# Performance work log

Measured on AMD Instinct MI355X. Metric: run time of the kernel, lower is better.

## Reference

```python
import jax, jax.numpy as jnp
import numpy as np

K = 16          # neighbors (init kwarg k)
LEAK = 0.2      # LeakyReLU slope
EPS = 1e-5      # GroupNorm eps
GROUPS = 4


def knn_idx(coor_k, coor_q, k):
    # coor_* : (B, 3, N); returns (B, Nq, k) indices of k nearest keys per query
    qk = jnp.einsum('bdq,bdk->bqk', coor_q, coor_k)
    q2 = jnp.sum(coor_q * coor_q, axis=1)[:, :, None]
    k2 = jnp.sum(coor_k * coor_k, axis=1)[:, None, :]
    d2 = q2 + k2 - 2.0 * qk                     # (B, Nq, Nk) squared distances
    _, idx = jax.lax.top_k(-d2, k)
    return idx


def gather_feats(x_k, idx):
    # x_k (B, D, Nk), idx (B, Nq, k) -> (B, D, Nq, k)
    feat = jax.vmap(lambda fk, i: fk[i])(jnp.transpose(x_k, (0, 2, 1)), idx)  # (B,Nq,k,D)
    return jnp.transpose(feat, (0, 3, 1, 2))


def graph_feature(coor_q, x_q, coor_k, x_k, k):
    idx = knn_idx(coor_k, coor_q, k)
    feat = gather_feats(x_k, idx)                # (B, D, Nq, k)
    xq = x_q[:, :, :, None]
    return jnp.concatenate([feat - xq, jnp.broadcast_to(xq, feat.shape)], axis=1)


def group_norm(x, gamma, beta):
    B, C, N, Kk = x.shape
    xg = x.reshape(B, GROUPS, C // GROUPS, N, Kk)
    mu = xg.mean(axis=(2, 3, 4), keepdims=True)
    var = xg.var(axis=(2, 3, 4), keepdims=True)
    xn = ((xg - mu) * jax.lax.rsqrt(var + EPS)).reshape(B, C, N, Kk)
    return xn * gamma[None, :, None, None] + beta[None, :, None, None]


def conv_gn_lrelu(x, w, gamma, beta):
    y = jnp.einsum('oc,bcnk->bonk', w, x)        # 1x1 conv, no bias
    y = group_norm(y, gamma, beta)
    return jnp.where(y > 0, y, LEAK * y)


def fps(xyz, npoint):
    # xyz (B, N, 3) -> (B, npoint) farthest-point-sampling indices, start at 0
    B, N, _ = xyz.shape
    d0 = jnp.full((B, N), 1e10, dtype=xyz.dtype)

    def step(carry, _):
        dist, far = carry
        centroid = jnp.take_along_axis(xyz, far[:, None, None], axis=1)  # (B,1,3)
        d = jnp.sum((xyz - centroid) ** 2, axis=-1)
        dist = jnp.minimum(dist, d)
        nxt = jnp.argmax(dist, axis=-1).astype(jnp.int32)
        return (dist, nxt), far

    far0 = jnp.zeros((B,), dtype=jnp.int32)
    _, idxs = jax.lax.scan(step, (d0, far0), None, length=npoint)
    return jnp.transpose(idxs)                   # (B, npoint)


def fps_downsample(coor, x, num_group):
    # coor (B,3,N), x (B,D,N)
    fidx = fps(jnp.transpose(coor, (0, 2, 1)), num_group)   # (B, num_group)
    comb = jnp.concatenate([coor, x], axis=1)                # (B, 3+D, N)
    new = jax.vmap(lambda c, i: c[:, i])(comb, fidx)         # (B, 3+D, num_group)
    return new[:, :3], new[:, 3:]


def setup_inputs() -> dict:
    key = jax.random.key(0)
    ks = jax.random.split(key, 8)
    B, N = 16, 2048
    return {
        'x': jax.random.normal(ks[0], (B, N, 3), jnp.float32),
        'num0': 512,
        'num1': 128,
        'w_in': jax.random.normal(ks[1], (8, 3), jnp.float32) * 0.3,
        'b_in': jax.random.normal(ks[2], (8,), jnp.float32) * 0.1,
        'w1': jax.random.normal(ks[3], (32, 16), jnp.float32) * 0.2,
        'g1': jnp.ones((32,), jnp.float32), 'be1': jnp.zeros((32,), jnp.float32),
        'w2': jax.random.normal(ks[4], (64, 64), jnp.float32) * 0.12,
        'g2': jnp.ones((64,), jnp.float32), 'be2': jnp.zeros((64,), jnp.float32),
        'w3': jax.random.normal(ks[5], (64, 128), jnp.float32) * 0.09,
        'g3': jnp.ones((64,), jnp.float32), 'be3': jnp.zeros((64,), jnp.float32),
        'w4': jax.random.normal(ks[6], (128, 128), jnp.float32) * 0.09,
        'g4': jnp.ones((128,), jnp.float32), 'be4': jnp.zeros((128,), jnp.float32),
    }


def reference(x, num0, num1, w_in, b_in, w1, g1, be1, w2, g2, be2,
              w3, g3, be3, w4, g4, be4):
    coor = jnp.transpose(x, (0, 2, 1))                       # (B,3,N)
    f = jnp.einsum('oc,bcn->bon', w_in, coor) + b_in[None, :, None]  # (B,8,N)

    f = graph_feature(coor, f, coor, f, K)                   # (B,16,N,K)
    f = conv_gn_lrelu(f, w1, g1, be1).max(axis=-1)           # (B,32,N)

    coor_q, f_q = fps_downsample(coor, f, num0)
    f = graph_feature(coor_q, f_q, coor, f, K)               # (B,64,num0,K)
    f = conv_gn_lrelu(f, w2, g2, be2).max(axis=-1)           # (B,64,num0)
    coor = coor_q

    f = graph_feature(coor, f, coor, f, K)                   # (B,128,num0,K)
    f = conv_gn_lrelu(f, w3, g3, be3).max(axis=-1)           # (B,64,num0)

    coor_q, f_q = fps_downsample(coor, f, num1)
    f = graph_feature(coor_q, f_q, coor, f, K)               # (B,128,num1,K)
    f = conv_gn_lrelu(f, w4, g4, be4).max(axis=-1)           # (B,128,num1)

    return jnp.transpose(coor_q, (0, 2, 1)), jnp.transpose(f, (0, 2, 1))
```

## Files before the change

kernel.cpp:

```cpp
#include <hip/hip_runtime.h>

#define KNN 16
static constexpr int BB = 16;
static constexpr float LEAK = 0.2f;
static constexpr float EPSV = 1e-5f;
typedef unsigned long long u64;

__device__ __forceinline__ void ce_asc(u64 &a, u64 &b) {
  u64 x = a, y = b; bool sw = y < x; a = sw ? y : x; b = sw ? x : y;
}
__device__ __forceinline__ void ce_desc(u64 &a, u64 &b) {
  u64 x = a, y = b; bool sw = x < y; a = sw ? y : x; b = sw ? x : y;
}
__device__ __forceinline__ void bitonic_sort16(u64 *T) {
#pragma unroll
  for (int k = 2; k <= 16; k <<= 1) {
#pragma unroll
    for (int j = k >> 1; j > 0; j >>= 1) {
#pragma unroll
      for (int i = 0; i < 16; ++i) {
        int l = i ^ j;
        if (l > i) {
          if ((i & k) == 0) ce_asc(T[i], T[l]); else ce_desc(T[i], T[l]);
        }
      }
    }
  }
}
__device__ __forceinline__ void merge_sorted16(u64 *R, const u64 *T) {
#pragma unroll
  for (int i = 0; i < 16; ++i) {
    u64 t = T[15 - i];
    R[i] = t < R[i] ? t : R[i];
  }
#pragma unroll
  for (int j = 8; j > 0; j >>= 1) {
#pragma unroll
    for (int i = 0; i < 16; ++i) {
      int l = i ^ j;
      if (l > i) ce_asc(R[i], R[l]);
    }
  }
}
template<int KC>
__device__ __forceinline__ void merge_row(const u64* __restrict__ p, u64* R) {
#pragma unroll
  for (int s = 0; s < 16; ++s) R[s] = p[s];
#pragma unroll
  for (int c = 1; c < KC; ++c) {
    u64 T[16];
#pragma unroll
    for (int s = 0; s < 16; ++s) T[s] = p[(size_t)c*KNN + s];
    merge_sorted16(R, T);
  }
}

__device__ __forceinline__ void f0_dev(const float* __restrict__ x,
    const float* __restrict__ w_in, const float* __restrict__ b_in,
    float* __restrict__ f0, int bid) {
  int i = bid * 256 + threadIdx.x;
  float px = x[i*3+0], py = x[i*3+1], pz = x[i*3+2];
#pragma unroll
  for (int o = 0; o < 8; ++o) {
    f0[i*8+o] = w_in[o*3+0]*px + w_in[o*3+1]*py + w_in[o*3+2]*pz + b_in[o];
  }
}

__device__ void knn_part_dev(const float* __restrict__ qxyz, int Nq,
    const float* __restrict__ kxyz, int Nk, int KC, u64* __restrict__ part,
    char* sm, int bid) {
  float4* keys = (float4*)sm;
  int nqb = (Nq + 255) >> 8;
  int c  = bid % KC;
  int qb = (bid / KC) % nqb;
  int b  = bid / (KC * nqb);
  int nkc = Nk / KC;
  int kbase = c * nkc;
  for (int j = threadIdx.x; j < nkc; j += 256) {
    const float* kp = kxyz + (size_t)(b*Nk + kbase + j)*3;
    float kx = kp[0], ky = kp[1], kz = kp[2];
    keys[j] = make_float4(kx, ky, kz, kx*kx + ky*ky + kz*kz);
  }
  __syncthreads();
  int q = (qb << 8) + threadIdx.x;
  if (q >= Nq) return;
  const float* qp = qxyz + (size_t)(b*Nq + q)*3;
  float qx = qp[0], qy = qp[1], qz = qp[2];
  float q2 = qx*qx + qy*qy + qz*qz;
  u64 R[16];
#pragma unroll
  for (int s = 0; s < 16; ++s) R[s] = 0xFFFFFFFFFFFFFFFFull;
  for (int j0 = 0; j0 < nkc; j0 += 16) {
    u64 T[16];
#pragma unroll
    for (int u = 0; u < 16; ++u) {
      float4 kk = keys[j0 + u];
      float qk = qx*kk.x + qy*kk.y + qz*kk.z;
      float d2 = q2 + kk.w - 2.0f*qk;
      int bb = __float_as_int(d2);
      unsigned k32 = (unsigned)bb ^ (unsigned)((bb >> 31) | 0x80000000);
      T[u] = ((u64)k32 << 32) | (unsigned)(kbase + j0 + u);
    }
    bitonic_sort16(T);
    merge_sorted16(R, T);
  }
  u64* op = part + ((size_t)(b*Nq + q)*KC + c)*KNN;
#pragma unroll
  for (int s = 0; s < KNN; ++s) op[s] = R[s];
}

__device__ __forceinline__ u64 fps_max64(u64 a, u64 b) { return a > b ? a : b; }
template<int CTRL>
__device__ __forceinline__ float fps_dpp_fmax(float v) {
  int nb = __builtin_amdgcn_update_dpp(0, __float_as_int(v), CTRL, 0xF, 0xF, false);
  return fmaxf(v, __int_as_float(nb));
}
template<int P, bool SAVE>
__device__ void fps_seg_dev(const float* __restrict__ xyz, int np,
    int t0, int t1, int* __restrict__ fidx,
    float* __restrict__ g_dl, int* __restrict__ g_far,
    int* __restrict__ inv, float* __restrict__ cq, char* sm, int b) {
  constexpr int NN = P * 256;
  float4* sc  = (float4*)sm;
  int* s_fid  = (int*)(sm + NN*16);
  u64* s_key  = (u64*)(sm + NN*16 + 2048);
  __builtin_amdgcn_s_setprio(1);
  int tid = threadIdx.x;
  int w = tid >> 6, lw = tid & 63;
  float px[P], py[P], pz[P], dl[P];
#pragma unroll
  for (int i = 0; i < P; ++i) {
    int p = tid * P + i;
    const float* pp = xyz + (size_t)(b*NN + p)*3;
    px[i] = pp[0]; py[i] = pp[1]; pz[i] = pp[2];
    sc[p] = make_float4(px[i], py[i], pz[i], 0.f);
  }
  int far;
  if (t0 == 0) {
#pragma unroll
    for (int i = 0; i < P; ++i) dl[i] = 1e10f;
    far = 0;
  } else {
#pragma unroll
    for (int i = 0; i < P; ++i) dl[i] = g_dl[b*NN + tid*P + i];
    far = g_far[b];
  }
  __syncthreads();
  for (int t = t0; t < t1; ++t) {
    if (tid == 0) { fidx[b*np + t] = far; s_fid[t] = far; }
    float4 cc = sc[far];
#pragma unroll
    for (int i = 0; i < P; ++i) {
      float dx = __fsub_rn(px[i], cc.x);
      float dy = __fsub_rn(py[i], cc.y);
      float dz = __fsub_rn(pz[i], cc.z);
      float d = __fadd_rn(__fadd_rn(__fmul_rn(dx,dx), __fmul_rn(dy,dy)), __fmul_rn(dz,dz));
      dl[i] = fminf(dl[i], d);
    }
    float m[P];
#pragma unroll
    for (int i = 0; i < P; ++i) m[i] = dl[i];
#pragma unroll
    for (int st = P/2; st > 0; st >>= 1) {
#pragma unroll
      for (int i = 0; i < P; ++i) if (i < st) m[i] = fmaxf(m[i], m[i + st]);
    }
    float lmax = m[0];
    unsigned msk = 0u;
#pragma unroll
    for (int i = 0; i < P; ++i) msk |= (dl[i] == lmax) ? (1u << i) : 0u;
    int lidx = tid * P + __builtin_ctz(msk);
    float v = lmax;
    v = fps_dpp_fmax<0x111>(v);
    v = fps_dpp_fmax<0x112>(v);
    v = fps_dpp_fmax<0x114>(v);
    v = fps_dpp_fmax<0x118>(v);
    v = fps_dpp_fmax<0x142>(v);
    v = fps_dpp_fmax<0x143>(v);
    float wmax = __int_as_float(__builtin_amdgcn_readlane(__float_as_int(v), 63));
    u64 bal = __ballot(lmax == wmax);
    int l0 = __ffsll((unsigned long long)bal) - 1;
    int wp = __builtin_amdgcn_readlane(lidx, l0);
    int buf = t & 1;
    if (lw == 0)
      s_key[buf*4 + w] = ((u64)__float_as_uint(wmax) << 32) | (unsigned)(~wp);
    __syncthreads();
    u64 best = s_key[buf*4 + 0];
    best = fps_max64(best, s_key[buf*4 + 1]);
    best = fps_max64(best, s_key[buf*4 + 2]);
    best = fps_max64(best, s_key[buf*4 + 3]);
    far = (int)(~(unsigned)(best & 0xFFFFFFFFull));
  }
  if constexpr (SAVE) {
#pragma unroll
    for (int i = 0; i < P; ++i) g_dl[b*NN + tid*P + i] = dl[i];
    if (tid == 0) g_far[b] = far;
  } else {
    __syncthreads();
    for (int j = tid; j < np; j += 256) {
      int p = (j >= t0) ? s_fid[j] : fidx[b*np + j];
      if (inv) inv[b*NN + p] = j;
      float4 c = sc[p];
      float* cp = cq + (size_t)(b*np + j)*3;
      cp[0] = c.x; cp[1] = c.y; cp[2] = c.z;
    }
  }
  __builtin_amdgcn_s_setprio(0);
}

__device__ __forceinline__ void fq1gather_dev(const float* __restrict__ f1,
    const int* __restrict__ fidx1, float* __restrict__ fq1, int bid) {
  int i = bid * 256 + threadIdx.x;
  int b = i >> 9;
  int src = fidx1[i];
  const float4* s = (const float4*)(f1 + (size_t)(b*2048 + src)*32);
  float4* d = (float4*)(fq1 + (size_t)i*32);
#pragma unroll
  for (int c = 0; c < 8; ++c) d[c] = s[c];
}

template<int C, int O, int QB, int KC, int NB>
__device__ void conv_dev(const float* __restrict__ fsrc, int Nsrc,
    const float* __restrict__ fq, int Nq, const u64* __restrict__ part,
    const float* __restrict__ w, float* __restrict__ ym, float* __restrict__ yn,
    double2* __restrict__ pp1, char* sm, int bid) {
  constexpr int Og = O / 4;
  constexpr int C4 = C / 4;
  double* rs  = (double*)sm;
  double* rs2 = rs + 256;
  float* ft   = (float*)(sm + 4096);
  float* fqs  = ft + QB*KNN*C;
  int* s_idx  = (int*)(fqs + QB*C);
  int tid = threadIdx.x;
  int chunk = bid % NB;
  int b = bid / NB;
  int q0 = chunk * QB;
  if (tid < QB) {
    const u64* p = part + (size_t)(b*Nq + q0 + tid)*KC*KNN;
    u64 R[16];
    merge_row<KC>(p, R);
#pragma unroll
    for (int s = 0; s < 16; ++s) s_idx[tid*KNN + s] = (int)(unsigned)(R[s] & 0xFFFFFFFFu);
  } else if (tid >= 64 && tid < 64 + QB*C4) {
    int t = tid - 64;
    int ql = t / C4, c4 = t % C4;
    ((float4*)&fqs[ql*C])[c4] = ((const float4*)(fq + (size_t)(b*Nq + q0 + ql)*C))[c4];
  }
  __syncthreads();
  for (int v = tid; v < QB*KNN*C4; v += 256) {
    int row = v / C4, c4 = v % C4;
    int ql = row / KNN, k = row % KNN;
    int src = s_idx[ql*KNN + k];
    ((float4*)&ft[(ql*KNN + k)*C])[c4] = ((const float4*)(fsrc + (size_t)(b*Nsrc + src)*C))[c4];
  }
  __syncthreads();
  int ql = tid / O, o = tid % O;
  float4 wr4[C4];
  float bs = 0.f;
  const float4* wp4 = (const float4*)(w + (size_t)o*2*C);
#pragma unroll
  for (int c4 = 0; c4 < C4; ++c4) {
    float4 lo = wp4[c4], hi = wp4[C4 + c4];
    float4 fv = ((const float4*)&fqs[ql*C])[c4];
    bs += (hi.x - lo.x) * fv.x;
    bs += (hi.y - lo.y) * fv.y;
    bs += (hi.z - lo.z) * fv.z;
    bs += (hi.w - lo.w) * fv.w;
    wr4[c4] = lo;
  }
  float mx = -3.4e38f, mn = 3.4e38f;
  double s = 0.0, s2 = 0.0;
  for (int k = 0; k < KNN; ++k) {
    float acc = bs;
    const float4* fv = (const float4*)&ft[(ql*KNN + k)*C];
#pragma unroll
    for (int c4 = 0; c4 < C4; ++c4) {
      float4 v = fv[c4];
      acc += wr4[c4].x*v.x; acc += wr4[c4].y*v.y;
      acc += wr4[c4].z*v.z; acc += wr4[c4].w*v.w;
    }
    mx = fmaxf(mx, acc);
    mn = fminf(mn, acc);
    s += acc;
    s2 += (double)acc * (double)acc;
  }
  size_t oidx = (size_t)(b*Nq + q0 + ql)*O + o;
  ym[oidx] = mx;
  yn[oidx] = mn;
  rs[tid] = s; rs2[tid] = s2;
  __syncthreads();
#pragma unroll
  for (int st = QB/2; st > 0; st >>= 1) {
    if (ql < st) { rs[tid] += rs[tid + st*O]; rs2[tid] += rs2[tid + st*O]; }
    __syncthreads();
  }
#pragma unroll
  for (int st = Og/2; st > 0; st >>= 1) {
    if (tid < O && (o % Og) < st) { rs[tid] += rs[tid + st]; rs2[tid] += rs2[tid + st]; }
    __syncthreads();
  }
  if (tid < O && (o % Og) == 0) {
    int g = o / Og;
    pp1[((size_t)b*NB + chunk)*4 + g] = make_double2(rs[tid], rs2[tid]);
  }
}

template<int O, int NB, int FCH, int NQ, int NSEL>
__device__ void fin_dev(const float* __restrict__ ym, const float* __restrict__ yn,
    const double2* __restrict__ pp1, const float* __restrict__ gamma,
    const float* __restrict__ beta, float* __restrict__ fout,
    const int* __restrict__ inv, float* __restrict__ fqout, char* sm, int bid) {
  constexpr int Og = O / 4;
  double* red  = (double*)sm;
  double* red2 = red + 64;
  float* s_mu  = (float*)(red2 + 64);
  float* s_rsv = s_mu + 4;
  int tid = threadIdx.x;
  int b = bid / FCH;
  int f = bid % FCH;
  if (tid < 64) {
    int g = tid >> 4, j = tid & 15;
    double s = 0.0, s2 = 0.0;
    for (int c = j; c < NB; c += 16) {
      double2 v = pp1[((size_t)b*NB + c)*4 + g];
      s += v.x; s2 += v.y;
    }
    red[tid] = s; red2[tid] = s2;
  }
  __syncthreads();
#pragma unroll
  for (int st = 8; st > 0; st >>= 1) {
    if (tid < 64 && (tid & 15) < st) { red[tid] += red[tid+st]; red2[tid] += red2[tid+st]; }
    __syncthreads();
  }
  if (tid < 4) {
    double cnt = (double)Og * (double)NQ * (double)KNN;
    double mu = red[tid*16] / cnt;
    double var = red2[tid*16] / cnt - mu*mu;
    s_mu[tid] = (float)mu;
    s_rsv[tid] = 1.0f / sqrtf((float)var + EPSV);
  }
  __syncthreads();
  constexpr int PER = NQ * O / FCH;
  int e0 = f * PER;
  for (int e = e0 + tid; e < e0 + PER; e += 256) {
    int q = e / O, o = e % O;
    int g = o / Og;
    size_t idx = (size_t)(b*NQ + q)*O + o;
    float ga = gamma[o], be = beta[o];
    float ysel = (ga >= 0.f) ? ym[idx] : yn[idx];
    float xn = (ysel - s_mu[g]) * s_rsv[g];
    float yv = xn*ga + be;
    yv = yv > 0.f ? yv : LEAK*yv;
    fout[idx] = yv;
    if constexpr (NSEL > 0) {
      int j = inv[b*NQ + q];
      if (j >= 0) fqout[(size_t)(b*NSEL + j)*O + o] = yv;
    }
  }
}

__global__ __launch_bounds__(256) void fusedA_kernel(const float* __restrict__ x,
    const float* __restrict__ w_in, const float* __restrict__ b_in,
    float* __restrict__ f0, u64* __restrict__ part, int* __restrict__ fidx1,
    float* __restrict__ g_dl, int* __restrict__ g_far) {
  extern __shared__ char sm[];
  int bid = blockIdx.x;
  if (bid < 16)        fps_seg_dev<8,true>(x, 512, 0, 280, fidx1, g_dl, g_far, nullptr, nullptr, sm, bid);
  else if (bid < 1040) knn_part_dev(x, 2048, x, 2048, 8, part, sm, bid - 16);
  else                 f0_dev(x, w_in, b_in, f0, bid - 1040);
}

__global__ __launch_bounds__(256) void conv1_kernel(const float* __restrict__ x,
    int* __restrict__ fidx1, float* __restrict__ g_dl, int* __restrict__ g_far,
    const float* __restrict__ f0, const u64* __restrict__ part,
    const float* __restrict__ w1, float* __restrict__ ym, float* __restrict__ yn,
    double2* __restrict__ pp1) {
  extern __shared__ char sm[];
  int bid = blockIdx.x;
  if (bid < 16) fps_seg_dev<8,true>(x, 512, 280, 460, fidx1, g_dl, g_far, nullptr, nullptr, sm, bid);
  else          conv_dev<8,32,8,8,256>(f0, 2048, f0, 2048, part, w1, ym, yn, pp1, sm, bid - 16);
}

__global__ __launch_bounds__(256) void fin1_kernel(const float* __restrict__ x,
    int* __restrict__ fidx1, float* __restrict__ g_dl, int* __restrict__ g_far,
    float* __restrict__ cq1,
    const float* __restrict__ ym, const float* __restrict__ yn,
    const double2* __restrict__ pp1, const float* __restrict__ g1,
    const float* __restrict__ be1, float* __restrict__ f1) {
  extern __shared__ char sm[];
  int bid = blockIdx.x;
  if (bid < 16) fps_seg_dev<8,false>(x, 512, 460, 512, fidx1, g_dl, g_far, nullptr, cq1, sm, bid);
  else          fin_dev<32,256,32,2048,0>(ym, yn, pp1, g1, be1, f1, nullptr, nullptr, sm, bid - 16);
}

__global__ __launch_bounds__(256) void fusedB_kernel(const float* __restrict__ cq1,
    const float* __restrict__ x, u64* __restrict__ part2, u64* __restrict__ part3,
    int* __restrict__ fidx2, float* __restrict__ g_dl, int* __restrict__ g_far,
    int* __restrict__ inv2, const float* __restrict__ f1, const int* __restrict__ fidx1,
    float* __restrict__ fq1) {
  extern __shared__ char sm[];
  int bid = blockIdx.x;
  if (bid < 16) {
    fps_seg_dev<2,true>(cq1, 128, 0, 100, fidx2, g_dl, g_far, nullptr, nullptr, sm, bid);
  } else if (bid < 272) {
    if (bid < 48) inv2[(bid - 16)*256 + threadIdx.x] = -1;
    knn_part_dev(cq1, 512, x, 2048, 8, part2, sm, bid - 16);
  } else if (bid < 528) {
    knn_part_dev(cq1, 512, cq1, 512, 8, part3, sm, bid - 272);
  } else {
    fq1gather_dev(f1, fidx1, fq1, bid - 528);
  }
}

__global__ __launch_bounds__(256) void conv2_kernel(const float* __restrict__ cq1,
    int* __restrict__ fidx2, float* __restrict__ g_dl, int* __restrict__ g_far,
    int* __restrict__ inv2, float* __restrict__ cq2,
    const float* __restrict__ f1, const float* __restrict__ fq1,
    const u64* __restrict__ part2, const float* __restrict__ w2,
    float* __restrict__ ym, float* __restrict__ yn, double2* __restrict__ pp1) {
  extern __shared__ char sm[];
  int bid = blockIdx.x;
  if (bid < 16) fps_seg_dev<2,false>(cq1, 128, 100, 128, fidx2, g_dl, g_far, inv2, cq2, sm, bid);
  else          conv_dev<32,64,4,8,128>(f1, 2048, fq1, 512, part2, w2, ym, yn, pp1, sm, bid - 16);
}

__global__ __launch_bounds__(256) void fin2_kernel(const float* __restrict__ ym,
    const float* __restrict__ yn, const double2* __restrict__ pp1,
    const float* __restrict__ g2, const float* __restrict__ be2,
    float* __restrict__ f2) {
  extern __shared__ char sm[];
  fin_dev<64,128,16,512,0>(ym, yn, pp1, g2, be2, f2, nullptr, nullptr, sm, blockIdx.x);
}

__global__ __launch_bounds__(256) void conv3k4_kernel(const float* __restrict__ cq2,
    const float* __restrict__ cq1, u64* __restrict__ part4,
    const float* __restrict__ f2, const u64* __restrict__ part3,
    const float* __restrict__ w3, float* __restrict__ ym, float* __restrict__ yn,
    double2* __restrict__ pp1) {
  extern __shared__ char sm[];
  int bid = blockIdx.x;
  if (bid < 128) knn_part_dev(cq2, 128, cq1, 512, 8, part4, sm, bid);
  else           conv_dev<64,64,4,8,128>(f2, 512, f2, 512, part3, w3, ym, yn, pp1, sm, bid - 128);
}

__global__ __launch_bounds__(256) void fin3_kernel(const float* __restrict__ ym,
    const float* __restrict__ yn, const double2* __restrict__ pp1,
    const float* __restrict__ g3, const float* __restrict__ be3,
    float* __restrict__ f3, const int* __restrict__ inv2, float* __restrict__ fq2) {
  extern __shared__ char sm[];
  fin_dev<64,128,16,512,128>(ym, yn, pp1, g3, be3, f3, inv2, fq2, sm, blockIdx.x);
}

__global__ __launch_bounds__(256) void conv4_kernel(const float* __restrict__ f3,
    const float* __restrict__ fq2, const u64* __restrict__ part4,
    const float* __restrict__ w4, float* __restrict__ ym, float* __restrict__ yn,
    double2* __restrict__ pp1) {
  extern __shared__ char sm[];
  conv_dev<64,128,2,8,64>(f3, 512, fq2, 128, part4, w4, ym, yn, pp1, sm, blockIdx.x);
}

__global__ __launch_bounds__(256) void fin4_kernel(const float* __restrict__ ym,
    const float* __restrict__ yn, const double2* __restrict__ pp1,
    const float* __restrict__ g4, const float* __restrict__ be4,
    float* __restrict__ f4) {
  extern __shared__ char sm[];
  fin_dev<128,64,8,128,0>(ym, yn, pp1, g4, be4, f4, nullptr, nullptr, sm, blockIdx.x);
}

extern "C" void kernel_launch(void* const* d_in, const int* in_sizes, int n_in,
                              void* d_out, int out_size, void* d_ws, size_t ws_size,
                              hipStream_t stream) {
  const float* x    = (const float*)d_in[0];
  const float* w_in = (const float*)d_in[3];
  const float* b_in = (const float*)d_in[4];
  const float* w1 = (const float*)d_in[5];
  const float* g1 = (const float*)d_in[6];
  const float* be1= (const float*)d_in[7];
  const float* w2 = (const float*)d_in[8];
  const float* g2 = (const float*)d_in[9];
  const float* be2= (const float*)d_in[10];
  const float* w3 = (const float*)d_in[11];
  const float* g3 = (const float*)d_in[12];
  const float* be3= (const float*)d_in[13];
  const float* w4 = (const float*)d_in[14];
  const float* g4 = (const float*)d_in[15];
  const float* be4= (const float*)d_in[16];
  float* out = (float*)d_out;
  (void)in_sizes; (void)n_in; (void)out_size; (void)ws_size;

  char* ws = (char*)d_ws;
  size_t off = 0;
  auto alloc = [&](size_t count) {
    void* p = ws + off;
    off += (count * 4 + 255) & ~(size_t)255;
    return p;
  };
  float* f0    = (float*)alloc(16*2048*8);
  float* f1    = (float*)alloc(16*2048*32);
  float* f2    = (float*)alloc(16*512*64);
  float* f3    = (float*)alloc(16*512*64);
  float* fq1   = (float*)alloc(16*512*32);
  float* fq2   = (float*)alloc(16*128*64);
  float* cq1   = (float*)alloc(16*512*3);
  float* ym    = (float*)alloc(16*2048*32);
  float* yn    = (float*)alloc(16*2048*32);
  double2* pp1 = (double2*)alloc(16*256*4*4);
  int* fidx1   = (int*)alloc(16*512);
  int* fidx2   = (int*)alloc(16*128);
  int* inv2    = (int*)alloc(16*512);
  float* g_dl1 = (float*)alloc(16*2048);
  int* g_far1  = (int*)alloc(16);
  float* g_dl2 = (float*)alloc(16*512);
  int* g_far2  = (int*)alloc(16);
  u64* part1 = (u64*)alloc((size_t)2 * 16*2048*8*16);
  u64* part2 = part1;
  u64* part3 = part1 + (size_t)16*512*8*16;
  u64* part4 = part1 + (size_t)2*16*512*8*16;

  float* cq2 = out;
  float* f4  = out + 16*128*3;

  constexpr size_t SM_F1  = 2048*16 + 2048 + 64;
  constexpr size_t SM_F2  = 512*16 + 2048 + 64;
  constexpr size_t SM_KNN = 4096;
  constexpr size_t SM_C1  = 4096 + 8*KNN*8*4 + 8*8*4 + 8*KNN*4;
  constexpr size_t SM_C2  = 4096 + 4*KNN*32*4 + 4*32*4 + 4*KNN*4;
  constexpr size_t SM_C3  = 4096 + 4*KNN*64*4 + 4*64*4 + 4*KNN*4;
  constexpr size_t SM_C4  = 4096 + 2*KNN*64*4 + 2*64*4 + 2*KNN*4;
  constexpr size_t SM_FIN = 1056;
  auto mx2 = [](size_t a, size_t b) { return a > b ? a : b; };

  fusedA_kernel<<<1168, 256, mx2(SM_F1, SM_KNN), stream>>>(x, w_in, b_in, f0, part1, fidx1, g_dl1, g_far1);
  conv1_kernel<<<4112, 256, mx2(SM_F1, SM_C1), stream>>>(x, fidx1, g_dl1, g_far1, f0, part1, w1, ym, yn, pp1);
  fin1_kernel<<<528, 256, mx2(SM_F1, SM_FIN), stream>>>(x, fidx1, g_dl1, g_far1, cq1, ym, yn, pp1, g1, be1, f1);

  fusedB_kernel<<<560, 256, mx2(SM_F2, SM_KNN), stream>>>(cq1, x, part2, part3, fidx2, g_dl2, g_far2, inv2, f1, fidx1, fq1);
  conv2_kernel<<<2064, 256, mx2(SM_F2, SM_C2), stream>>>(cq1, fidx2, g_dl2, g_far2, inv2, cq2, f1, fq1, part2, w2, ym, yn, pp1);
  fin2_kernel<<<256, 256, SM_FIN, stream>>>(ym, yn, pp1, g2, be2, f2);

  conv3k4_kernel<<<2176, 256, mx2(SM_KNN, SM_C3), stream>>>(cq2, cq1, part4, f2, part3, w3, ym, yn, pp1);
  fin3_kernel<<<256, 256, SM_FIN, stream>>>(ym, yn, pp1, g3, be3, f3, inv2, fq2);

  conv4_kernel<<<1024, 256, SM_C4, stream>>>(f3, fq2, part4, w4, ym, yn, pp1);
  fin4_kernel<<<128, 256, SM_FIN, stream>>>(ym, yn, pp1, g4, be4, f4);
}
```

Before: 470.5 us.

## Run second FPS stage in a single wavefront without block barriers

```diff
diff --git a/kernel.cpp b/kernel.cpp
--- a/kernel.cpp
+++ b/kernel.cpp
@@ -115,11 +115,14 @@
   int nb = __builtin_amdgcn_update_dpp(0, __float_as_int(v), CTRL, 0xF, 0xF, false);
   return fmaxf(v, __int_as_float(nb));
 }
+__device__ __forceinline__ float rl_f(float v, int l) {
+  return __int_as_float(__builtin_amdgcn_readlane(__float_as_int(v), l));
+}
 template<int P, bool SAVE>
 __device__ void fps_seg_dev(const float* __restrict__ xyz, int np,
     int t0, int t1, int* __restrict__ fidx,
     float* __restrict__ g_dl, int* __restrict__ g_far,
-    int* __restrict__ inv, float* __restrict__ cq, char* sm, int b) {
+    float* __restrict__ cq, char* sm, int b) {
   constexpr int NN = P * 256;
   float4* sc  = (float4*)sm;
   int* s_fid  = (int*)(sm + NN*16);
@@ -147,7 +150,7 @@
   }
   __syncthreads();
   for (int t = t0; t < t1; ++t) {
-    if (tid == 0) { fidx[b*np + t] = far; s_fid[t] = far; }
+    if (tid == 0) s_fid[t] = far;
     float4 cc = sc[far];
 #pragma unroll
     for (int i = 0; i < P; ++i) {
@@ -177,7 +180,7 @@
     v = fps_dpp_fmax<0x118>(v);
     v = fps_dpp_fmax<0x142>(v);
     v = fps_dpp_fmax<0x143>(v);
-    float wmax = __int_as_float(__builtin_amdgcn_readlane(__float_as_int(v), 63));
+    float wmax = rl_f(v, 63);
     u64 bal = __ballot(lmax == wmax);
     int l0 = __ffsll((unsigned long long)bal) - 1;
     int wp = __builtin_amdgcn_readlane(lidx, l0);
@@ -191,18 +194,107 @@
     best = fps_max64(best, s_key[buf*4 + 3]);
     far = (int)(~(unsigned)(best & 0xFFFFFFFFull));
   }
+  for (int t = t0 + tid; t < t1; t += 256) fidx[b*np + t] = s_fid[t];
   if constexpr (SAVE) {
 #pragma unroll
     for (int i = 0; i < P; ++i) g_dl[b*NN + tid*P + i] = dl[i];
     if (tid == 0) g_far[b] = far;
   } else {
-    __syncthreads();
     for (int j = tid; j < np; j += 256) {
       int p = (j >= t0) ? s_fid[j] : fidx[b*np + j];
-      if (inv) inv[b*NN + p] = j;
       float4 c = sc[p];
       float* cp = cq + (size_t)(b*np + j)*3;
       cp[0] = c.x; cp[1] = c.y; cp[2] = c.z;
+    }
+  }
+  __builtin_amdgcn_s_setprio(0);
+}
+
+template<int P, bool SAVE>
+__device__ void fps2_wave_dev(const float* __restrict__ xyz, int np,
+    int t0, int t1, int* __restrict__ fidx,
+    float* __restrict__ g_dl, int* __restrict__ g_far,
+    int* __restrict__ inv, float* __restrict__ cq, char* sm, int b) {
+  constexpr int NN = P * 64;
+  int* s_fid = (int*)sm;
+  __builtin_amdgcn_s_setprio(1);
+  int l = threadIdx.x;
+  float px[P], py[P], pz[P], dl[P];
+#pragma unroll
+  for (int i = 0; i < P; ++i) {
+    int p = l * P + i;
+    const float* pp = xyz + (size_t)(b*NN + p)*3;
+    px[i] = pp[0]; py[i] = pp[1]; pz[i] = pp[2];
+  }
+  int far;
+  if (t0 == 0) {
+#pragma unroll
+    for (int i = 0; i < P; ++i) dl[i] = 1e10f;
+    far = 0;
+  } else {
+#pragma unroll
+    for (int i = 0; i < P; ++i) dl[i] = g_dl[b*NN + l*P + i];
+    far = g_far[b];
+  }
+  const float* fp = xyz + (size_t)(b*NN + far)*3;
+  float ccx = fp[0], ccy = fp[1], ccz = fp[2];
+  for (int t = t0; t < t1; ++t) {
+    if (l == 0) s_fid[t] = far;
+#pragma unroll
+    for (int i = 0; i < P; ++i) {
+      float dx = __fsub_rn(px[i], ccx);
+      float dy = __fsub_rn(py[i], ccy);
+      float dz = __fsub_rn(pz[i], ccz);
+      float d = __fadd_rn(__fadd_rn(__fmul_rn(dx,dx), __fmul_rn(dy,dy)), __fmul_rn(dz,dz));
+      dl[i] = fminf(dl[i], d);
+    }
+    float m[P];
+#pragma unroll
+    for (int i = 0; i < P; ++i) m[i] = dl[i];
+#pragma unroll
+    for (int st = P/2; st > 0; st >>= 1) {
+#pragma unroll
+      for (int i = 0; i < P; ++i) if (i < st) m[i] = fmaxf(m[i], m[i + st]);
+    }
+    float lmax = m[0];
+    unsigned msk = 0u;
+#pragma unroll
+    for (int i = 0; i < P; ++i) msk |= (dl[i] == lmax) ? (1u << i) : 0u;
+    int ib = __builtin_ctz(msk);
+    int lidx = l * P + ib;
+    float cxl = px[P-1], cyl = py[P-1], czl = pz[P-1];
+#pragma unroll
+    for (int i = P-1; i >= 0; --i) {
+      bool tk = (msk >> i) & 1u;
+      cxl = tk ? px[i] : cxl;
+      cyl = tk ? py[i] : cyl;
+      czl = tk ? pz[i] : czl;
+    }
+    float v = lmax;
+    v = fps_dpp_fmax<0x111>(v);
+    v = fps_dpp_fmax<0x112>(v);
+    v = fps_dpp_fmax<0x114>(v);
+    v = fps_dpp_fmax<0x118>(v);
+    v = fps_dpp_fmax<0x142>(v);
+    v = fps_dpp_fmax<0x143>(v);
+    float wmax = rl_f(v, 63);
+    u64 bal = __ballot(lmax == wmax);
+    int l0 = __ffsll((unsigned long long)bal) - 1;
+    far = __builtin_amdgcn_readlane(lidx, l0);
+    ccx = rl_f(cxl, l0); ccy = rl_f(cyl, l0); ccz = rl_f(czl, l0);
+  }
+  for (int t = t0 + l; t < t1; t += 64) fidx[b*np + t] = s_fid[t];
+  if constexpr (SAVE) {
+#pragma unroll
+    for (int i = 0; i < P; ++i) g_dl[b*NN + l*P + i] = dl[i];
+    if (l == 0) g_far[b] = far;
+  } else {
+    for (int j = l; j < np; j += 64) {
+      int p = (j >= t0) ? s_fid[j] : fidx[b*np + j];
+      if (inv) inv[b*NN + p] = j;
+      const float* sp = xyz + (size_t)(b*NN + p)*3;
+      float* cp = cq + (size_t)(b*np + j)*3;
+      cp[0] = sp[0]; cp[1] = sp[1]; cp[2] = sp[2];
     }
   }
   __builtin_amdgcn_s_setprio(0);
@@ -366,7 +458,7 @@
     float* __restrict__ g_dl, int* __restrict__ g_far) {
   extern __shared__ char sm[];
   int bid = blockIdx.x;
-  if (bid < 16)        fps_seg_dev<8,true>(x, 512, 0, 280, fidx1, g_dl, g_far, nullptr, nullptr, sm, bid);
+  if (bid < 16)        fps_seg_dev<8,true>(x, 512, 0, 280, fidx1, g_dl, g_far, nullptr, sm, bid);
   else if (bid < 1040) knn_part_dev(x, 2048, x, 2048, 8, part, sm, bid - 16);
   else                 f0_dev(x, w_in, b_in, f0, bid - 1040);
 }
@@ -378,7 +470,7 @@
     double2* __restrict__ pp1) {
   extern __shared__ char sm[];
   int bid = blockIdx.x;
-  if (bid < 16) fps_seg_dev<8,true>(x, 512, 280, 460, fidx1, g_dl, g_far, nullptr, nullptr, sm, bid);
+  if (bid < 16) fps_seg_dev<8,true>(x, 512, 280, 460, fidx1, g_dl, g_far, nullptr, sm, bid);
   else          conv_dev<8,32,8,8,256>(f0, 2048, f0, 2048, part, w1, ym, yn, pp1, sm, bid - 16);
 }
 
@@ -390,7 +482,7 @@
     const float* __restrict__ be1, float* __restrict__ f1) {
   extern __shared__ char sm[];
   int bid = blockIdx.x;
-  if (bid < 16) fps_seg_dev<8,false>(x, 512, 460, 512, fidx1, g_dl, g_far, nullptr, cq1, sm, bid);
+  if (bid < 16) fps_seg_dev<8,false>(x, 512, 460, 512, fidx1, g_dl, g_far, cq1, sm, bid);
   else          fin_dev<32,256,32,2048,0>(ym, yn, pp1, g1, be1, f1, nullptr, nullptr, sm, bid - 16);
 }
 
@@ -402,7 +494,8 @@
   extern __shared__ char sm[];
   int bid = blockIdx.x;
   if (bid < 16) {
-    fps_seg_dev<2,true>(cq1, 128, 0, 100, fidx2, g_dl, g_far, nullptr, nullptr, sm, bid);
+    if (threadIdx.x < 64)
+      fps2_wave_dev<8,true>(cq1, 128, 0, 100, fidx2, g_dl, g_far, nullptr, nullptr, sm, bid);
   } else if (bid < 272) {
     if (bid < 48) inv2[(bid - 16)*256 + threadIdx.x] = -1;
     knn_part_dev(cq1, 512, x, 2048, 8, part2, sm, bid - 16);
@@ -421,8 +514,11 @@
     float* __restrict__ ym, float* __restrict__ yn, double2* __restrict__ pp1) {
   extern __shared__ char sm[];
   int bid = blockIdx.x;
-  if (bid < 16) fps_seg_dev<2,false>(cq1, 128, 100, 128, fidx2, g_dl, g_far, inv2, cq2, sm, bid);
-  else          conv_dev<32,64,4,8,128>(f1, 2048, fq1, 512, part2, w2, ym, yn, pp1, sm, bid - 16);
+  if (bid < 16) {
+    if (threadIdx.x < 64)
+      fps2_wave_dev<8,false>(cq1, 128, 100, 128, fidx2, g_dl, g_far, inv2, cq2, sm, bid);
+  }
+  else conv_dev<32,64,4,8,128>(f1, 2048, fq1, 512, part2, w2, ym, yn, pp1, sm, bid - 16);
 }
 
 __global__ __launch_bounds__(256) void fin2_kernel(const float* __restrict__ ym,
@@ -522,7 +618,7 @@
   float* f4  = out + 16*128*3;
 
   constexpr size_t SM_F1  = 2048*16 + 2048 + 64;
-  constexpr size_t SM_F2  = 512*16 + 2048 + 64;
+  constexpr size_t SM_F2W = 512;
   constexpr size_t SM_KNN = 4096;
   constexpr size_t SM_C1  = 4096 + 8*KNN*8*4 + 8*8*4 + 8*KNN*4;
   constexpr size_t SM_C2  = 4096 + 4*KNN*32*4 + 4*32*4 + 4*KNN*4;
@@ -535,8 +631,8 @@
   conv1_kernel<<<4112, 256, mx2(SM_F1, SM_C1), stream>>>(x, fidx1, g_dl1, g_far1, f0, part1, w1, ym, yn, pp1);
   fin1_kernel<<<528, 256, mx2(SM_F1, SM_FIN), stream>>>(x, fidx1, g_dl1, g_far1, cq1, ym, yn, pp1, g1, be1, f1);
 
-  fusedB_kernel<<<560, 256, mx2(SM_F2, SM_KNN), stream>>>(cq1, x, part2, part3, fidx2, g_dl2, g_far2, inv2, f1, fidx1, fq1);
-  conv2_kernel<<<2064, 256, mx2(SM_F2, SM_C2), stream>>>(cq1, fidx2, g_dl2, g_far2, inv2, cq2, f1, fq1, part2, w2, ym, yn, pp1);
+  fusedB_kernel<<<560, 256, mx2(SM_F2W, SM_KNN), stream>>>(cq1, x, part2, part3, fidx2, g_dl2, g_far2, inv2, f1, fidx1, fq1);
+  conv2_kernel<<<2064, 256, mx2(SM_F2W, SM_C2), stream>>>(cq1, fidx2, g_dl2, g_far2, inv2, cq2, f1, fq1, part2, w2, ym, yn, pp1);
   fin2_kernel<<<256, 256, SM_FIN, stream>>>(ym, yn, pp1, g2, be2, f2);
 
   conv3k4_kernel<<<2176, 256, mx2(SM_KNN, SM_C3), stream>>>(cq2, cq1, part4, f2, part3, w3, ym, yn, pp1);
```

Result: no change. 475.4 us (+1.0%).
